# Kernel optimization log

Measured on AMD Instinct MI355X. Metric: run time of the kernel, lower is better.

The kernel has to match this reference:

```python
import jax, jax.numpy as jnp
import numpy as np

ALPHA = 0.5
WIN_SIZE = 31
BN_EPS = 1e-5
LRELU_SLOPE = 0.1


def setup_inputs() -> dict:
    key = jax.random.key(0)
    k1, k2, k3, k4 = jax.random.split(key, 4)
    B, N, C, P, E = 4, 2048, 64, 48, 128
    return {
        "sig_new": jax.random.normal(k1, (B, N, C, P), dtype=jnp.float32),
        "atten_mem": jax.random.normal(k2, (B, N, C, P), dtype=jnp.float32),
        "conv_w": jax.random.normal(k3, (E, C, P), dtype=jnp.float32) * 0.05,
        "conv_b": jax.random.normal(k4, (E,), dtype=jnp.float32) * 0.05,
        "bn_gamma": jnp.ones((E,), dtype=jnp.float32),
        "bn_beta": jnp.zeros((E,), dtype=jnp.float32),
    }


def _neighbour_mask(n_cutout):
    # clamped banded mask (pano_scan=False / training-mode branch)
    half = WIN_SIZE // 2
    cols = jnp.clip(jnp.arange(n_cutout)[:, None] + jnp.arange(-half, half + 1)[None, :], 0, n_cutout - 1)
    rows = jnp.broadcast_to(jnp.arange(n_cutout)[:, None], cols.shape)
    return jnp.zeros((n_cutout, n_cutout), jnp.float32).at[rows, cols].set(1.0)


def _embed(x, conv_w, conv_b, bn_gamma, bn_beta, B, N):
    # Conv1d(kernel=n_pts) on length-n_pts input == full contraction over (c, p)
    y = jnp.einsum("ncp,ecp->ne", x.reshape(-1, x.shape[-2], x.shape[-1]), conv_w) + conv_b
    # BatchNorm1d, training-mode batch statistics over the (B*N) batch dim
    mu = y.mean(axis=0)
    var = ((y - mu) ** 2).mean(axis=0)
    y = (y - mu) * jax.lax.rsqrt(var + BN_EPS) * bn_gamma + bn_beta
    y = jnp.where(y >= 0, y, LRELU_SLOPE * y)  # LeakyReLU(0.1)
    return y.reshape(B, N, -1)


def reference(sig_new, atten_mem, conv_w, conv_b, bn_gamma, bn_beta):
    B, N, C, P = sig_new.shape
    mask = _neighbour_mask(N)
    embed_x = _embed(sig_new, conv_w, conv_b, bn_gamma, bn_beta, B, N)      # [B,N,E]
    embed_t = _embed(atten_mem, conv_w, conv_b, bn_gamma, bn_beta, B, N)    # [B,N,E]
    sim = jnp.einsum("bie,bje->bij", embed_x, embed_t)                      # [B,N,N]
    sim = sim - 1e10 * (1.0 - mask)
    mx = jnp.max(sim, axis=-1, keepdims=True)
    ex = jnp.exp(sim - mx) * mask
    attn = ex / jnp.sum(ex, axis=-1, keepdims=True)                          # [B,N,N]
    mem_flat = atten_mem.reshape(B, N, C * P)
    mem_w = jnp.einsum("bij,bjf->bif", attn, mem_flat).reshape(B, N, C, P)
    new_mem = ALPHA * sig_new + (1.0 - ALPHA) * mem_w
    return new_mem, attn
```

## Files before the change

kernel.cpp:

```cpp
#include <hip/hip_runtime.h>

#define BATCH 4
#define NDIM 2048
#define EDIM 128
#define KDIM 3072
#define MDIM 8192
#define HALF 15

typedef __attribute__((ext_vector_type(8))) short short8v;
typedef __attribute__((ext_vector_type(4))) float f32x4;

__device__ inline ushort bf16h(float x) {
  union { float f; unsigned u; } v; v.f = x;
  unsigned r = v.u + 0x7fff + ((v.u >> 16) & 1);
  return (ushort)(r >> 16);
}

__global__ __launch_bounds__(256)
void k_wprep(const float* __restrict__ w, ushort* __restrict__ wh, ushort* __restrict__ wl) {
  const int q = (blockIdx.x * 256 + threadIdx.x) * 4;
  float4 v = *(const float4*)(w + q);
  const float f[4] = {v.x, v.y, v.z, v.w};
  ushort4 h, l;
  ushort* ph = (ushort*)&h; ushort* pl = (ushort*)&l;
#pragma unroll
  for (int j = 0; j < 4; ++j) {
    unsigned u = __float_as_uint(f[j]);
    ph[j] = (ushort)(u >> 16);
    pl[j] = bf16h(f[j] - __uint_as_float(u & 0xffff0000u));
  }
  *(ushort4*)(wh + q) = h;
  *(ushort4*)(wl + q) = l;
}

#define BMT 128
#define BK 32

__global__ __launch_bounds__(256, 2)
void k_gemm(const float* __restrict__ x0, const float* __restrict__ x1,
            const ushort* __restrict__ wh, const ushort* __restrict__ wl,
            float* __restrict__ part, int splitK) {
  const int tid = threadIdx.x;
  const int m0 = blockIdx.x * BMT;
  const int kc = blockIdx.y;
  const int inp = blockIdx.z;
  const float* __restrict__ x = inp ? x1 : x0;
  const int kpc = KDIM / splitK;
  const int kbeg = kc * kpc;
  const int nsteps = kpc / BK;

  __shared__ ushort sAh[BMT][BK];
  __shared__ ushort sAl[BMT][BK];
  __shared__ ushort sBh[EDIM][BK];
  __shared__ ushort sBl[EDIM][BK];

  const int mrow = tid >> 3;
  const int c4 = (tid & 7) << 2;

  const int lane = tid & 63;
  const int wid = tid >> 6;
  const int wr = wid >> 1;
  const int wc = wid & 1;
  const int fr = lane & 15;
  const int kg = (lane >> 4) << 3;

  f32x4 acc[4][4];
#pragma unroll
  for (int a = 0; a < 4; ++a)
#pragma unroll
    for (int b = 0; b < 4; ++b) acc[a][b] = (f32x4){0.f, 0.f, 0.f, 0.f};

  float4 rA[4];
  ushort4 rBh[4], rBl[4];
  {
    const float* xb = x + (size_t)(m0 + mrow) * KDIM + kbeg + c4;
    const ushort* wb = wh + (size_t)mrow * KDIM + kbeg + c4;
    const ushort* wb2 = wl + (size_t)mrow * KDIM + kbeg + c4;
#pragma unroll
    for (int i = 0; i < 4; ++i) {
      rA[i]  = *(const float4*)(xb + (size_t)(32 * i) * KDIM);
      rBh[i] = *(const ushort4*)(wb + (size_t)(32 * i) * KDIM);
      rBl[i] = *(const ushort4*)(wb2 + (size_t)(32 * i) * KDIM);
    }
  }

  for (int st = 0; st < nsteps; ++st) {
    __syncthreads();
#pragma unroll
    for (int i = 0; i < 4; ++i) {
      const int m = mrow + 32 * i;
      const float fa[4] = {rA[i].x, rA[i].y, rA[i].z, rA[i].w};
      ushort4 ah, al;
      ushort* pah = (ushort*)&ah; ushort* pal = (ushort*)&al;
#pragma unroll
      for (int j = 0; j < 4; ++j) {
        unsigned u = __float_as_uint(fa[j]);
        pah[j] = (ushort)(u >> 16);
        pal[j] = bf16h(fa[j] - __uint_as_float(u & 0xffff0000u));
      }
      *(ushort4*)&sAh[m][c4] = ah;
      *(ushort4*)&sAl[m][c4] = al;
      *(ushort4*)&sBh[m][c4] = rBh[i];
      *(ushort4*)&sBl[m][c4] = rBl[i];
    }
    __syncthreads();

    if (st + 1 < nsteps) {
      const int ko = kbeg + (st + 1) * BK + c4;
      const float* xb = x + (size_t)(m0 + mrow) * KDIM + ko;
      const ushort* wb = wh + (size_t)mrow * KDIM + ko;
      const ushort* wb2 = wl + (size_t)mrow * KDIM + ko;
#pragma unroll
      for (int i = 0; i < 4; ++i) {
        rA[i]  = *(const float4*)(xb + (size_t)(32 * i) * KDIM);
        rBh[i] = *(const ushort4*)(wb + (size_t)(32 * i) * KDIM);
        rBl[i] = *(const ushort4*)(wb2 + (size_t)(32 * i) * KDIM);
      }
    }

    short8v ah[4], al[4], bh[4], bl[4];
#pragma unroll
    for (int mi = 0; mi < 4; ++mi) {
      const int row = wr * 64 + mi * 16 + fr;
      ah[mi] = *(const short8v*)&sAh[row][kg];
      al[mi] = *(const short8v*)&sAl[row][kg];
    }
#pragma unroll
    for (int ei = 0; ei < 4; ++ei) {
      const int e = wc * 64 + ei * 16 + fr;
      bh[ei] = *(const short8v*)&sBh[e][kg];
      bl[ei] = *(const short8v*)&sBl[e][kg];
    }
#pragma unroll
    for (int mi = 0; mi < 4; ++mi)
#pragma unroll
      for (int ei = 0; ei < 4; ++ei) {
        acc[mi][ei] = __builtin_amdgcn_mfma_f32_16x16x32_bf16(ah[mi], bh[ei], acc[mi][ei], 0, 0, 0);
        acc[mi][ei] = __builtin_amdgcn_mfma_f32_16x16x32_bf16(ah[mi], bl[ei], acc[mi][ei], 0, 0, 0);
        acc[mi][ei] = __builtin_amdgcn_mfma_f32_16x16x32_bf16(al[mi], bh[ei], acc[mi][ei], 0, 0, 0);
      }
  }

  float* po = part + ((size_t)(inp * splitK + kc) * MDIM + m0) * EDIM;
#pragma unroll
  for (int mi = 0; mi < 4; ++mi) {
    const int mloc = wr * 64 + mi * 16 + ((lane >> 4) << 2);
#pragma unroll
    for (int ei = 0; ei < 4; ++ei) {
      const int e = wc * 64 + ei * 16 + fr;
#pragma unroll
      for (int r = 0; r < 4; ++r)
        po[(size_t)(mloc + r) * EDIM + e] = acc[mi][ei][r];
    }
  }
}

__global__ __launch_bounds__(256)
void k_reduce(const float* __restrict__ part, const float* __restrict__ bvec,
              float* __restrict__ y, float* __restrict__ spart, int splitK) {
  const int tid = threadIdx.x;
  const int in = blockIdx.z;
  const int rb = blockIdx.x;
  const int e = tid & 127;
  const int rh = tid >> 7;
  const float bb = bvec[e];
  float s = 0.f, s2 = 0.f;
  for (int rr = 0; rr < 32; ++rr) {
    const int r = rb * 64 + rh * 32 + rr;
    float v = 0.f;
    for (int kc = 0; kc < splitK; ++kc)
      v += part[((size_t)(in * splitK + kc) * MDIM + r) * EDIM + e];
    v += bb;
    y[((size_t)in * MDIM + r) * EDIM + e] = v;
    s += v; s2 += v * v;
  }
  __shared__ float l1[256], l2[256];
  l1[tid] = s; l2[tid] = s2;
  __syncthreads();
  if (rh == 0) {
    s = l1[e] + l1[e + 128];
    s2 = l2[e] + l2[e + 128];
    spart[((size_t)(in * 128 + rb) * 2 + 0) * 128 + e] = s;
    spart[((size_t)(in * 128 + rb) * 2 + 1) * 128 + e] = s2;
  }
}

__global__ void k_finalize(const float* __restrict__ spart, const float* __restrict__ gamma,
                           const float* __restrict__ beta, float* __restrict__ scsh) {
  const int in = blockIdx.x;
  const int e = threadIdx.x;
  float s = 0.f, s2 = 0.f;
  for (int rb = 0; rb < 128; ++rb) {
    s  += spart[((size_t)(in * 128 + rb) * 2 + 0) * 128 + e];
    s2 += spart[((size_t)(in * 128 + rb) * 2 + 1) * 128 + e];
  }
  const float mu = s * (1.f / MDIM);
  const float var = s2 * (1.f / MDIM) - mu * mu;
  const float rs = rsqrtf(var + 1e-5f);
  const float sc = gamma[e] * rs;
  const float sh = beta[e] - mu * sc;
  scsh[in * 128 + e] = sc;
  scsh[256 + in * 128 + e] = sh;
}

__global__ __launch_bounds__(256)
void k_bnapply(float* __restrict__ y, const float* __restrict__ scsh) {
  int q = blockIdx.x * 256 + threadIdx.x;
  float4* yv = (float4*)y;
#pragma unroll
  for (int it = 0; it < 2; ++it, q += 262144) {
    float4 v = yv[q];
    const int in = q >> 18;
    const int e0 = (q & 31) << 2;
    const float* sc = scsh + in * 128 + e0;
    const float* sh = scsh + 256 + in * 128 + e0;
    float t;
    t = fmaf(sc[0], v.x, sh[0]); v.x = t >= 0.f ? t : 0.1f * t;
    t = fmaf(sc[1], v.y, sh[1]); v.y = t >= 0.f ? t : 0.1f * t;
    t = fmaf(sc[2], v.z, sh[2]); v.z = t >= 0.f ? t : 0.1f * t;
    t = fmaf(sc[3], v.w, sh[3]); v.w = t >= 0.f ? t : 0.1f * t;
    yv[q] = v;
  }
}

__global__ __launch_bounds__(256)
void k_sim(const float* __restrict__ y, float* __restrict__ attn, float* __restrict__ aw) {
  const int tid = threadIdx.x;
  const int row = blockIdx.x * 4 + (tid >> 6);
  const int lane = tid & 63;
  const int b = row >> 11;
  const int i = row & 2047;
  const int jlo = max(0, i - HALF);
  const int jhi = min(NDIM - 1, i + HALF);
  const int j = jlo + lane;
  const bool valid = (lane < 31) && (j <= jhi);
  const int jc = valid ? j : jlo;
  const float* __restrict__ xr = y + (size_t)row * EDIM;
  const float* __restrict__ tr = y + (size_t)MDIM * EDIM + ((size_t)(b << 11) + jc) * EDIM;
  float s = 0.f;
#pragma unroll
  for (int e = 0; e < EDIM; e += 4) {
    float4 u = *(const float4*)(xr + e);
    float4 v = *(const float4*)(tr + e);
    s = fmaf(u.x, v.x, s); s = fmaf(u.y, v.y, s);
    s = fmaf(u.z, v.z, s); s = fmaf(u.w, v.w, s);
  }
  float sm = valid ? s : -1e30f;
  float mx = sm;
#pragma unroll
  for (int o = 1; o < 64; o <<= 1) mx = fmaxf(mx, __shfl_xor(mx, o));
  const float p = valid ? __expf(sm - mx) : 0.f;
  float ss = p;
#pragma unroll
  for (int o = 1; o < 64; o <<= 1) ss += __shfl_xor(ss, o);
  const float a = p / ss;

  float* orow = attn + (size_t)row * NDIM;
  const int bw = jhi - jlo;
  for (int c0 = lane << 2; c0 < NDIM; c0 += 256) {
    float4 v;
    float* pv = (float*)&v;
#pragma unroll
    for (int t = 0; t < 4; ++t) {
      const int d = c0 + t - jlo;
      const float val = __shfl(a, d & 63);
      pv[t] = (d >= 0 && d <= bw) ? val : 0.f;
    }
    *(float4*)(orow + c0) = v;
  }
  if (lane < 32) aw[(size_t)row * 32 + lane] = valid ? a : 0.f;
}

#define TI 16
#define TJMAX 46
#define FC 256
#define NIT (NDIM / TI)
#define NFC (KDIM / FC)
#define NWG_MEMW (NIT * NFC * BATCH)

__global__ __launch_bounds__(256, 2)
void k_memw(const float* __restrict__ sig, const float* __restrict__ mem,
            const float* __restrict__ aw, float* __restrict__ out) {
  const int tid = threadIdx.x;
  const int bid = blockIdx.x;
  const int nid = (bid & 7) * (NWG_MEMW / 8) + (bid >> 3);
  const int b  = nid / (NIT * NFC);
  const int r  = nid % (NIT * NFC);
  const int fc0 = (r / NIT) * FC;
  const int i0  = (r % NIT) * TI;
  const int jlo = max(0, i0 - HALF);
  const int jhi = min(NDIM - 1, i0 + TI - 1 + HALF);
  const int tj = jhi - jlo + 1;

  __shared__ float sV[TJMAX][FC];
  __shared__ float sWt[TJMAX][TI];

  for (int idx = tid; idx < tj * TI; idx += 256) {
    const int jj = idx >> 4;
    const int ii = idx & 15;
    const int ii_g = i0 + ii;
    const int jg = jlo + jj;
    const int jli = max(0, ii_g - HALF);
    const int jhii = min(NDIM - 1, ii_g + HALF);
    float wv = 0.f;
    if (jg >= jli && jg <= jhii) wv = aw[(size_t)((b << 11) + ii_g) * 32 + (jg - jli)];
    sWt[jj][ii] = wv;
  }
  for (int idx = tid; idx < tj * (FC / 4); idx += 256) {
    const int jj = idx >> 6;
    const int f4 = idx & 63;
    *(float4*)&sV[jj][f4 << 2] =
        *(const float4*)(mem + (size_t)((b << 11) + jlo + jj) * KDIM + fc0 + (f4 << 2));
  }
  __syncthreads();

  const int ig = tid >> 6;
  const int fg = tid & 63;
  const int ibase = i0 + (ig << 2);
  const int wlo = max(jlo, ibase - HALF) - jlo;
  const int whi = min(jhi, ibase + 3 + HALF) - jlo;

  float acc[4][4];
#pragma unroll
  for (int a = 0; a < 4; ++a)
#pragma unroll
    for (int c = 0; c < 4; ++c) acc[a][c] = 0.f;

  for (int jj = wlo; jj <= whi; ++jj) {
    float4 wv = *(const float4*)&sWt[jj][ig << 2];
    float4 vv = *(const float4*)&sV[jj][fg << 2];
    const float wa[4] = {wv.x, wv.y, wv.z, wv.w};
    const float va[4] = {vv.x, vv.y, vv.z, vv.w};
#pragma unroll
    for (int mi = 0; mi < 4; ++mi)
#pragma unroll
      for (int fi = 0; fi < 4; ++fi)
        acc[mi][fi] = fmaf(wa[mi], va[fi], acc[mi][fi]);
  }

  const size_t base = (size_t)((b << 11) + ibase) * KDIM + fc0 + (fg << 2);
#pragma unroll
  for (int mi = 0; mi < 4; ++mi) {
    float4 sv = *(const float4*)(sig + base + (size_t)mi * KDIM);
    float4 ov;
    ov.x = 0.5f * sv.x + 0.5f * acc[mi][0];
    ov.y = 0.5f * sv.y + 0.5f * acc[mi][1];
    ov.z = 0.5f * sv.z + 0.5f * acc[mi][2];
    ov.w = 0.5f * sv.w + 0.5f * acc[mi][3];
    *(float4*)(out + base + (size_t)mi * KDIM) = ov;
  }
}

extern "C" void kernel_launch(void* const* d_in, const int* in_sizes, int n_in,
                              void* d_out, int out_size, void* d_ws, size_t ws_size,
                              hipStream_t stream) {
  const float* sig   = (const float*)d_in[0];
  const float* mem   = (const float*)d_in[1];
  const float* w     = (const float*)d_in[2];
  const float* bv    = (const float*)d_in[3];
  const float* gamma = (const float*)d_in[4];
  const float* beta  = (const float*)d_in[5];

  float* out_mem  = (float*)d_out;
  float* out_attn = out_mem + (size_t)BATCH * NDIM * KDIM;

  float* wsf = (float*)d_ws;
  const size_t ME = (size_t)MDIM * EDIM;
  const size_t fixed = 2 * ME + 65536 + 512 + 262144 + 196608;
  int splitK = 4;
  while (splitK > 1 && ((size_t)2 * splitK * ME + fixed) * 4 > ws_size) splitK >>= 1;

  float* part  = wsf;
  float* y     = part + (size_t)2 * splitK * ME;
  float* spart = y + 2 * ME;
  float* scsh  = spart + 65536;
  float* aw    = scsh + 512;
  ushort* wh   = (ushort*)(aw + 262144);
  ushort* wl   = wh + (size_t)EDIM * KDIM;

  hipLaunchKernelGGL(k_wprep, dim3(EDIM * KDIM / 1024), dim3(256), 0, stream, w, wh, wl);

  dim3 g1(MDIM / BMT, splitK, 2);
  hipLaunchKernelGGL(k_gemm, g1, dim3(256), 0, stream, sig, mem, wh, wl, part, splitK);

  dim3 g2(MDIM / 64, 1, 2);
  hipLaunchKernelGGL(k_reduce, g2, dim3(256), 0, stream, part, bv, y, spart, splitK);

  hipLaunchKernelGGL(k_finalize, dim3(2), dim3(128), 0, stream, spart, gamma, beta, scsh);

  hipLaunchKernelGGL(k_bnapply, dim3(1024), dim3(256), 0, stream, y, scsh);

  hipLaunchKernelGGL(k_sim, dim3(MDIM / 4), dim3(256), 0, stream, y, out_attn, aw);

  hipLaunchKernelGGL(k_memw, dim3(NWG_MEMW), dim3(256), 0, stream, sig, mem, aw, out_mem);
}
```

Baseline: 477.1 us.

## Fuse BN/LeakyReLU into similarity kernel with LDS tiles; halve GEMM M-tile

Removes the separate BN-apply pass and applies scale/shift plus LeakyReLU while loading embedding rows into shared memory in the similarity kernel. Each block now stages its four query rows and the shared window of key rows in LDS, so neighbouring rows reuse the same key rows. Separately, the split-K GEMM M tile shrinks from 128 to 64 rows and launch bounds allow four blocks per CU, raising occupancy at the cost of more reloads of the weight tile.

```diff
diff --git a/kernel.cpp b/kernel.cpp
--- a/kernel.cpp
+++ b/kernel.cpp
@@ -33,10 +33,10 @@
   *(ushort4*)(wl + q) = l;
 }
 
-#define BMT 128
+#define BMT 64
 #define BK 32
 
-__global__ __launch_bounds__(256, 2)
+__global__ __launch_bounds__(256, 4)
 void k_gemm(const float* __restrict__ x0, const float* __restrict__ x1,
             const ushort* __restrict__ wh, const ushort* __restrict__ wl,
             float* __restrict__ part, int splitK) {
@@ -64,21 +64,23 @@
   const int fr = lane & 15;
   const int kg = (lane >> 4) << 3;
 
-  f32x4 acc[4][4];
-#pragma unroll
-  for (int a = 0; a < 4; ++a)
+  f32x4 acc[2][4];
+#pragma unroll
+  for (int a = 0; a < 2; ++a)
 #pragma unroll
     for (int b = 0; b < 4; ++b) acc[a][b] = (f32x4){0.f, 0.f, 0.f, 0.f};
 
-  float4 rA[4];
+  float4 rA[2];
   ushort4 rBh[4], rBl[4];
   {
     const float* xb = x + (size_t)(m0 + mrow) * KDIM + kbeg + c4;
     const ushort* wb = wh + (size_t)mrow * KDIM + kbeg + c4;
     const ushort* wb2 = wl + (size_t)mrow * KDIM + kbeg + c4;
 #pragma unroll
+    for (int i = 0; i < 2; ++i)
+      rA[i] = *(const float4*)(xb + (size_t)(32 * i) * KDIM);
+#pragma unroll
     for (int i = 0; i < 4; ++i) {
-      rA[i]  = *(const float4*)(xb + (size_t)(32 * i) * KDIM);
       rBh[i] = *(const ushort4*)(wb + (size_t)(32 * i) * KDIM);
       rBl[i] = *(const ushort4*)(wb2 + (size_t)(32 * i) * KDIM);
     }
@@ -87,7 +89,7 @@
   for (int st = 0; st < nsteps; ++st) {
     __syncthreads();
 #pragma unroll
-    for (int i = 0; i < 4; ++i) {
+    for (int i = 0; i < 2; ++i) {
       const int m = mrow + 32 * i;
       const float fa[4] = {rA[i].x, rA[i].y, rA[i].z, rA[i].w};
       ushort4 ah, al;
@@ -100,6 +102,10 @@
       }
       *(ushort4*)&sAh[m][c4] = ah;
       *(ushort4*)&sAl[m][c4] = al;
+    }
+#pragma unroll
+    for (int i = 0; i < 4; ++i) {
+      const int m = mrow + 32 * i;
       *(ushort4*)&sBh[m][c4] = rBh[i];
       *(ushort4*)&sBl[m][c4] = rBl[i];
     }
@@ -111,17 +117,19 @@
       const ushort* wb = wh + (size_t)mrow * KDIM + ko;
       const ushort* wb2 = wl + (size_t)mrow * KDIM + ko;
 #pragma unroll
+      for (int i = 0; i < 2; ++i)
+        rA[i] = *(const float4*)(xb + (size_t)(32 * i) * KDIM);
+#pragma unroll
       for (int i = 0; i < 4; ++i) {
-        rA[i]  = *(const float4*)(xb + (size_t)(32 * i) * KDIM);
         rBh[i] = *(const ushort4*)(wb + (size_t)(32 * i) * KDIM);
         rBl[i] = *(const ushort4*)(wb2 + (size_t)(32 * i) * KDIM);
       }
     }
 
-    short8v ah[4], al[4], bh[4], bl[4];
-#pragma unroll
-    for (int mi = 0; mi < 4; ++mi) {
-      const int row = wr * 64 + mi * 16 + fr;
+    short8v ah[2], al[2], bh[4], bl[4];
+#pragma unroll
+    for (int mi = 0; mi < 2; ++mi) {
+      const int row = wr * 32 + mi * 16 + fr;
       ah[mi] = *(const short8v*)&sAh[row][kg];
       al[mi] = *(const short8v*)&sAl[row][kg];
     }
@@ -132,7 +140,7 @@
       bl[ei] = *(const short8v*)&sBl[e][kg];
     }
 #pragma unroll
-    for (int mi = 0; mi < 4; ++mi)
+    for (int mi = 0; mi < 2; ++mi)
 #pragma unroll
       for (int ei = 0; ei < 4; ++ei) {
         acc[mi][ei] = __builtin_amdgcn_mfma_f32_16x16x32_bf16(ah[mi], bh[ei], acc[mi][ei], 0, 0, 0);
@@ -143,8 +151,8 @@
 
   float* po = part + ((size_t)(inp * splitK + kc) * MDIM + m0) * EDIM;
 #pragma unroll
-  for (int mi = 0; mi < 4; ++mi) {
-    const int mloc = wr * 64 + mi * 16 + ((lane >> 4) << 2);
+  for (int mi = 0; mi < 2; ++mi) {
+    const int mloc = wr * 32 + mi * 16 + ((lane >> 4) << 2);
 #pragma unroll
     for (int ei = 0; ei < 4; ++ei) {
       const int e = wc * 64 + ei * 16 + fr;
@@ -203,45 +211,63 @@
   scsh[256 + in * 128 + e] = sh;
 }
 
+#define SIMW 34
+#define SIMP 132
+
 __global__ __launch_bounds__(256)
-void k_bnapply(float* __restrict__ y, const float* __restrict__ scsh) {
-  int q = blockIdx.x * 256 + threadIdx.x;
-  float4* yv = (float4*)y;
-#pragma unroll
-  for (int it = 0; it < 2; ++it, q += 262144) {
-    float4 v = yv[q];
-    const int in = q >> 18;
-    const int e0 = (q & 31) << 2;
-    const float* sc = scsh + in * 128 + e0;
-    const float* sh = scsh + 256 + in * 128 + e0;
-    float t;
-    t = fmaf(sc[0], v.x, sh[0]); v.x = t >= 0.f ? t : 0.1f * t;
-    t = fmaf(sc[1], v.y, sh[1]); v.y = t >= 0.f ? t : 0.1f * t;
-    t = fmaf(sc[2], v.z, sh[2]); v.z = t >= 0.f ? t : 0.1f * t;
-    t = fmaf(sc[3], v.w, sh[3]); v.w = t >= 0.f ? t : 0.1f * t;
-    yv[q] = v;
-  }
-}
-
-__global__ __launch_bounds__(256)
-void k_sim(const float* __restrict__ y, float* __restrict__ attn, float* __restrict__ aw) {
+void k_sim(const float* __restrict__ y, const float* __restrict__ scsh,
+           float* __restrict__ attn, float* __restrict__ aw) {
   const int tid = threadIdx.x;
-  const int row = blockIdx.x * 4 + (tid >> 6);
+  const int bid = blockIdx.x;
+  const int b = bid >> 9;
+  const int i0 = (bid << 2) & 2047;
+  const int jlo = max(0, i0 - HALF);
+  const int jhi = min(NDIM - 1, i0 + 3 + HALF);
+  const int tw = jhi - jlo + 1;
+
+  __shared__ float sT[SIMW][SIMP];
+  __shared__ float sX[4][SIMP];
+  __shared__ float sSc[2][128], sSh[2][128];
+
+  if (tid < 128) { sSc[0][tid] = scsh[tid]; sSh[0][tid] = scsh[256 + tid]; }
+  else { const int e = tid - 128; sSc[1][e] = scsh[128 + e]; sSh[1][e] = scsh[384 + e]; }
+  __syncthreads();
+
+  const int totq = (4 + tw) * 32;
+  for (int q = tid; q < totq; q += 256) {
+    const int rr = q >> 5;
+    const int e4 = (q & 31) << 2;
+    const bool isx = rr < 4;
+    const int gr = isx ? ((b << 11) + i0 + rr)
+                       : (MDIM + (b << 11) + jlo + (rr - 4));
+    float4 v = *(const float4*)(y + (size_t)gr * EDIM + e4);
+    const float* sc = isx ? sSc[0] : sSc[1];
+    const float* sh = isx ? sSh[0] : sSh[1];
+    const float* pv = (const float*)&v;
+    float* dst = isx ? &sX[rr][e4] : &sT[rr - 4][e4];
+#pragma unroll
+    for (int t = 0; t < 4; ++t) {
+      const float val = fmaf(sc[e4 + t], pv[t], sh[e4 + t]);
+      dst[t] = val >= 0.f ? val : 0.1f * val;
+    }
+  }
+  __syncthreads();
+
   const int lane = tid & 63;
-  const int b = row >> 11;
-  const int i = row & 2047;
-  const int jlo = max(0, i - HALF);
-  const int jhi = min(NDIM - 1, i + HALF);
-  const int j = jlo + lane;
-  const bool valid = (lane < 31) && (j <= jhi);
-  const int jc = valid ? j : jlo;
-  const float* __restrict__ xr = y + (size_t)row * EDIM;
-  const float* __restrict__ tr = y + (size_t)MDIM * EDIM + ((size_t)(b << 11) + jc) * EDIM;
+  const int wv = tid >> 6;
+  const int i = i0 + wv;
+  const int row = (b << 11) + i;
+  const int jliw = max(0, i - HALF);
+  const int jhiw = min(NDIM - 1, i + HALF);
+  const int j = jliw + lane;
+  const bool valid = (lane < 31) && (j <= jhiw);
+  const int trow = (valid ? j : jliw) - jlo;
+
   float s = 0.f;
 #pragma unroll
   for (int e = 0; e < EDIM; e += 4) {
-    float4 u = *(const float4*)(xr + e);
-    float4 v = *(const float4*)(tr + e);
+    float4 u = *(const float4*)&sX[wv][e];
+    float4 v = *(const float4*)&sT[trow][e];
     s = fmaf(u.x, v.x, s); s = fmaf(u.y, v.y, s);
     s = fmaf(u.z, v.z, s); s = fmaf(u.w, v.w, s);
   }
@@ -256,13 +282,13 @@
   const float a = p / ss;
 
   float* orow = attn + (size_t)row * NDIM;
-  const int bw = jhi - jlo;
+  const int bw = jhiw - jliw;
   for (int c0 = lane << 2; c0 < NDIM; c0 += 256) {
     float4 v;
     float* pv = (float*)&v;
 #pragma unroll
     for (int t = 0; t < 4; ++t) {
-      const int d = c0 + t - jlo;
+      const int d = c0 + t - jliw;
       const float val = __shfl(a, d & 63);
       pv[t] = (d >= 0 && d <= bw) ? val : 0.f;
     }
@@ -388,9 +414,7 @@
 
   hipLaunchKernelGGL(k_finalize, dim3(2), dim3(128), 0, stream, spart, gamma, beta, scsh);
 
-  hipLaunchKernelGGL(k_bnapply, dim3(1024), dim3(256), 0, stream, y, scsh);
-
-  hipLaunchKernelGGL(k_sim, dim3(MDIM / 4), dim3(256), 0, stream, y, out_attn, aw);
+  hipLaunchKernelGGL(k_sim, dim3(MDIM / 4), dim3(256), 0, stream, y, scsh, out_attn, aw);
 
   hipLaunchKernelGGL(k_memw, dim3(NWG_MEMW), dim3(256), 0, stream, sig, mem, aw, out_mem);
 }
```

Measured after the change: 474.0 us. No clear change (-0.7%).
